# Optimization experiments

Hardware: AMD Instinct MI355X
Metric: run time of the kernel (lower is better)

## Reference

```python
import jax, jax.numpy as jnp
import numpy as np

B, D, T_STEPS = 256, 512, 64


def setup_inputs() -> dict:
    key = jax.random.key(0)
    ks = jax.random.split(key, 9)
    s = 1.0 / np.sqrt(D)  # torch LSTM init scale
    return {
        "h": jax.random.normal(ks[0], (B, D), dtype=jnp.float32),
        "T": T_STEPS,
        "W_ih0": jax.random.uniform(ks[1], (4 * D, D), jnp.float32, -s, s),
        "W_hh0": jax.random.uniform(ks[2], (4 * D, D), jnp.float32, -s, s),
        "b_ih0": jax.random.uniform(ks[3], (4 * D,), jnp.float32, -s, s),
        "b_hh0": jax.random.uniform(ks[4], (4 * D,), jnp.float32, -s, s),
        "W_ih1": jax.random.uniform(ks[5], (4 * D, D), jnp.float32, -s, s),
        "W_hh1": jax.random.uniform(ks[6], (4 * D, D), jnp.float32, -s, s),
        "b_ih1": jax.random.uniform(ks[7], (4 * D,), jnp.float32, -s, s),
        "b_hh1": jax.random.uniform(ks[8], (4 * D,), jnp.float32, -s, s),
    }


def _lstm_cell(x, h, c, W_ih, W_hh, b_ih, b_hh):
    # gates: [B, 4D], torch gate order (i, f, g, o)
    gates = x @ W_ih.T + h @ W_hh.T + (b_ih + b_hh)
    i, f, g, o = jnp.split(gates, 4, axis=-1)
    c_new = jax.nn.sigmoid(f) * c + jax.nn.sigmoid(i) * jnp.tanh(g)
    h_new = jax.nn.sigmoid(o) * jnp.tanh(c_new)
    return h_new, c_new


def reference(h, T, W_ih0, W_hh0, b_ih0, b_hh0, W_ih1, W_hh1, b_ih1, b_hh1):
    b, d = h.shape
    zeros = jnp.zeros((b, d), dtype=h.dtype)

    def step(carry, _):
        x, h0, c0, h1, c1 = carry
        h0, c0 = _lstm_cell(x, h0, c0, W_ih0, W_hh0, b_ih0, b_hh0)
        h1, c1 = _lstm_cell(h0, h1, c1, W_ih1, W_hh1, b_ih1, b_hh1)
        # output of layer 2 is fed back as next step's input
        return (h1, h0, c0, h1, c1), h1

    init = (h, zeros, zeros, zeros, zeros)
    _, e_seq = jax.lax.scan(step, init, xs=None, length=T)
    return e_seq  # [T, B, D]
```

## Files before the change

### kernel.cpp

```cpp
#include <hip/hip_runtime.h>


#define BD    131072
#define SMEM_WBYTES 131072
#define SMEM_BYTES  (SMEM_WBYTES + 4 * 1056 * 4)

#define WS_SLOTS 0
#define WS_XINIT 4096
#define WS_ZERO  (WS_XINIT + BD * 2)
#define WS_ROT   (WS_ZERO + BD * 2)
#define ROT_BYTES ((size_t)BD * 2)
#define WS_NEED_DEEP (WS_ROT + 128 * ROT_BYTES)
#define WS_NEED_RING (WS_ROT + 4 * ROT_BYTES)

typedef _Float16 half8_t  __attribute__((ext_vector_type(8)));
typedef float    f32x16_t __attribute__((ext_vector_type(16)));
typedef float    f32x4_t  __attribute__((ext_vector_type(4)));

#define LOADC(p)  __hip_atomic_load((p), __ATOMIC_RELAXED, __HIP_MEMORY_SCOPE_AGENT)
#define STOREC(p, v) __hip_atomic_store((p), (v), __ATOMIC_RELAXED, __HIP_MEMORY_SCOPE_AGENT)

__device__ __forceinline__ float sigmoidf_(float x) {
  float z = __expf(-fabsf(x));
  float s = 1.0f / (1.0f + z);
  return x >= 0.0f ? s : 1.0f - s;
}
__device__ __forceinline__ float tanhf_(float x) {
  float z = __expf(-2.0f * fabsf(x));
  float t = (1.0f - z) / (1.0f + z);
  return x >= 0.0f ? t : -t;
}

__device__ __forceinline__ f32x4_t load_cv16(const void* p) {
  f32x4_t r;
  asm volatile("global_load_dwordx4 %0, %1, off sc0 sc1"
               : "=v"(r) : "v"(p) : "memory");
  return r;
}

__global__ void lstm_init(const float* __restrict__ h, char* __restrict__ ws) {
  int i = blockIdx.x * 256 + threadIdx.x;
  unsigned* slots = (unsigned*)(ws + WS_SLOTS);
  _Float16* xinit = (_Float16*)(ws + WS_XINIT);
  _Float16* zerob = (_Float16*)(ws + WS_ZERO);
  if (i < BD) {
    xinit[i] = (_Float16)h[i];
    zerob[i] = (_Float16)0.0f;
  }
  if (i < 256) slots[i] = 0u;
}

__global__ void __launch_bounds__(256, 1) lstm_persist(
    const float* __restrict__ Wih0, const float* __restrict__ Whh0,
    const float* __restrict__ bih0, const float* __restrict__ bhh0,
    const float* __restrict__ Wih1, const float* __restrict__ Whh1,
    const float* __restrict__ bih1, const float* __restrict__ bhh1,
    float* __restrict__ out, char* __restrict__ ws, int deep)
{
  extern __shared__ char smem[];
  float* red = (float*)(smem + SMEM_WBYTES);
  unsigned* slots = (unsigned*)(ws + WS_SLOTS);
  const _Float16* xinit = (const _Float16*)(ws + WS_XINIT);
  const _Float16* zerob = (const _Float16*)(ws + WS_ZERO);
  char* rot = ws + WS_ROT;

  const int tid = threadIdx.x;
  const int l = tid & 63;
  const int w = tid >> 6;
  const int bid = blockIdx.x;
  const int bb = (bid & 7) >> 1;
  const int db = ((bid >> 3) << 1) | (bid & 1);
  const int b0 = bb << 6;
  const int d0 = db << 3;

#pragma unroll
  for (int L = 0; L < 2; ++L) {
    for (int it = 0; it < 16; ++it) {
      int slot = it * 256 + tid;
      int s2 = slot >> 6, lane = slot & 63;
      int khalf = s2 >> 5, ks = s2 & 31;
      int kg = lane >> 5, nl = lane & 31;
      int ng = ((nl >> 3) << 9) + d0 + (nl & 7);
      int col = ks * 16 + kg * 8;
      const float* srcb = khalf ? (L ? Whh1 : Whh0) : (L ? Wih1 : Wih0);
      const float* src = srcb + (size_t)ng * 512 + col;
      half8_t hv;
#pragma unroll
      for (int j = 0; j < 8; ++j) hv[j] = (_Float16)src[j];
      *(half8_t*)(smem + (size_t)L * 65536 + (size_t)slot * 16) = hv;
    }
  }

  const int cbl = tid >> 2;
  const int j0 = (tid & 3) << 1;
  float bias0[4][2], bias1[4][2];
#pragma unroll
  for (int g = 0; g < 4; ++g) {
#pragma unroll
    for (int p = 0; p < 2; ++p) {
      int ng = (g << 9) + d0 + j0 + p;
      bias0[g][p] = bih0[ng] + bhh0[ng];
      bias1[g][p] = bih1[ng] + bhh1[ng];
    }
  }
  float c0s[2] = {0.0f, 0.0f}, c1s[2] = {0.0f, 0.0f};
  unsigned* gflags = slots + (bb << 6);
  __syncthreads();

  for (int s = 0; s < 128; ++s) {
    const int t = s >> 1;
    const int layer = s & 1;
    const int fi = deep ? (s - 1) : ((s - 1) & 3);
    const int si = deep ? (s - 2) : ((s - 2) & 3);
    const int oi = deep ? s : (s & 3);
    const _Float16* fresh = (s == 0) ? xinit
                          : (const _Float16*)(rot + (size_t)fi * ROT_BYTES);
    const _Float16* stale = (s <= 1) ? zerob
                          : (const _Float16*)(rot + (size_t)si * ROT_BYTES);
    _Float16* hout = (_Float16*)(rot + (size_t)oi * ROT_BYTES);

    if (w < 2 && s > 0) {
      const unsigned* sl = gflags + l;
      unsigned v;
      do {
        v = LOADC(sl);
      } while (!__all((int)(v >= (unsigned)s)));
      asm volatile("" ::: "memory");
    }

    const _Float16* asrc = (w >= 2) ? stale : fresh;
    const char* ap = (const char*)(asrc + (size_t)(b0 + ((w & 1) << 5) + (l & 31)) * 512
                                        + ((l >> 5) << 3));
    int boff = layer * 65536 + ((w >> 1) * 32768) + l * 16;

    f32x16_t acc0, acc1;
#pragma unroll
    for (int r = 0; r < 16; ++r) { acc0[r] = 0.0f; acc1[r] = 0.0f; }

    if (deep) {
#pragma unroll
      for (int half = 0; half < 2; ++half) {
        f32x4_t va[16];
#pragma unroll
        for (int j = 0; j < 16; ++j)
          va[j] = *(const f32x4_t*)(ap + half * 512 + 32 * j);
#pragma unroll
        for (int ks = 0; ks < 8; ++ks) {
          half8_t a0  = __builtin_bit_cast(half8_t, va[2 * ks]);
          half8_t a1  = __builtin_bit_cast(half8_t, va[2 * ks + 1]);
          half8_t bv0 = *(const half8_t*)(smem + boff);
          half8_t bv1 = *(const half8_t*)(smem + boff + 1024);
          acc0 = __builtin_amdgcn_mfma_f32_32x32x16_f16(a0, bv0, acc0, 0, 0, 0);
          acc1 = __builtin_amdgcn_mfma_f32_32x32x16_f16(a1, bv1, acc1, 0, 0, 0);
          boff += 2048;
        }
      }
    } else {
#pragma unroll
      for (int half = 0; half < 2; ++half) {
        f32x4_t va[16];
#pragma unroll
        for (int j = 0; j < 16; ++j) va[j] = load_cv16(ap + half * 512 + 32 * j);
        asm volatile("s_waitcnt vmcnt(0)" ::: "memory");
#pragma unroll
        for (int ks = 0; ks < 8; ++ks) {
          half8_t a0  = __builtin_bit_cast(half8_t, va[2 * ks]);
          half8_t a1  = __builtin_bit_cast(half8_t, va[2 * ks + 1]);
          half8_t bv0 = *(const half8_t*)(smem + boff);
          half8_t bv1 = *(const half8_t*)(smem + boff + 1024);
          acc0 = __builtin_amdgcn_mfma_f32_32x32x16_f16(a0, bv0, acc0, 0, 0, 0);
          acc1 = __builtin_amdgcn_mfma_f32_32x32x16_f16(a1, bv1, acc1, 0, 0, 0);
          boff += 2048;
        }
      }
    }

    {
      float* redw = red + w * 1056 + (l & 31);
      const int rbase = (l >> 5) << 2;
#pragma unroll
      for (int r = 0; r < 16; ++r) {
        int row = (r & 3) + ((r >> 2) << 3) + rbase;
        redw[row * 33] = acc0[r] + acc1[r];
      }
    }
    __syncthreads();

    float hv[2];
    int gidx;
    {
      const int base = (cbl >> 5) * 1056 + (cbl & 31) * 33 + j0;
#pragma unroll
      for (int p = 0; p < 2; ++p) {
        float vi = red[base + p]      + red[base + 2112 + p]      + (layer ? bias1[0][p] : bias0[0][p]);
        float vf = red[base + 8 + p]  + red[base + 2112 + 8 + p]  + (layer ? bias1[1][p] : bias0[1][p]);
        float vg = red[base + 16 + p] + red[base + 2112 + 16 + p] + (layer ? bias1[2][p] : bias0[2][p]);
        float vo = red[base + 24 + p] + red[base + 2112 + 24 + p] + (layer ? bias1[3][p] : bias0[3][p]);
        float iv = sigmoidf_(vi), fv = sigmoidf_(vf);
        float gv = tanhf_(vg),    ov = sigmoidf_(vo);
        float cold = layer ? c1s[p] : c0s[p];
        float c = fv * cold + iv * gv;
        if (layer) c1s[p] = c; else c0s[p] = c;
        hv[p] = ov * tanhf_(c);
      }
      gidx = (b0 + cbl) * 512 + d0 + j0;
      unsigned hu = ((unsigned)__builtin_bit_cast(unsigned short, (_Float16)hv[0])) |
                    ((unsigned)__builtin_bit_cast(unsigned short, (_Float16)hv[1]) << 16);
      STOREC((unsigned*)&hout[gidx], hu);
    }
    asm volatile("s_waitcnt vmcnt(0)" ::: "memory");
    __syncthreads();
    if (tid == 0)
      STOREC(gflags + db, (unsigned)(s + 1));
    if (layer) {
      float* op = out + (size_t)t * BD + gidx;
      op[0] = hv[0]; op[1] = hv[1];
    }
  }
}

extern "C" void kernel_launch(void* const* d_in, const int* in_sizes, int n_in,
                              void* d_out, int out_size, void* d_ws, size_t ws_size,
                              hipStream_t stream) {
  const float* h    = (const float*)d_in[0];
  const float* Wih0 = (const float*)d_in[2];
  const float* Whh0 = (const float*)d_in[3];
  const float* bih0 = (const float*)d_in[4];
  const float* bhh0 = (const float*)d_in[5];
  const float* Wih1 = (const float*)d_in[6];
  const float* Whh1 = (const float*)d_in[7];
  const float* bih1 = (const float*)d_in[8];
  const float* bhh1 = (const float*)d_in[9];
  float* out = (float*)d_out;
  char* ws = (char*)d_ws;

  int deep = (ws_size >= (size_t)WS_NEED_DEEP) ? 1 : 0;

  hipFuncSetAttribute((const void*)lstm_persist,
                      hipFuncAttributeMaxDynamicSharedMemorySize, SMEM_BYTES);

  lstm_init<<<512, 256, 0, stream>>>(h, ws);

  void* args[] = { &Wih0, &Whh0, &bih0, &bhh0, &Wih1, &Whh1, &bih1, &bhh1,
                   &out, &ws, &deep };
  hipLaunchCooperativeKernel((void*)lstm_persist, dim3(256), dim3(256),
                             args, SMEM_BYTES, stream);
}
```

Baseline: 1.127 ms.

## Replace flag-based inter-block sync with sentinel-poisoned data polling

Drops the per-step flag counters and the spin-wait on them. The init kernel fills the whole 128-slot history buffer with an all-ones sentinel, and consumer waves poll the fresh h data itself until no word equals the sentinel. Each step therefore needs one round of global traffic instead of a flag store followed by a data load. The shallow ring-buffer fallback and the cooperative launch are removed. This relies on valid fp16 pairs never encoding 0xFFFFFFFF, adds an init pass that writes the full 32MB buffer, and skips work entirely if the workspace is too small.

```diff
diff --git a/kernel.cpp b/kernel.cpp
--- a/kernel.cpp
+++ b/kernel.cpp
@@ -5,19 +5,17 @@
 #define SMEM_WBYTES 131072
 #define SMEM_BYTES  (SMEM_WBYTES + 4 * 1056 * 4)
 
-#define WS_SLOTS 0
 #define WS_XINIT 4096
 #define WS_ZERO  (WS_XINIT + BD * 2)
 #define WS_ROT   (WS_ZERO + BD * 2)
 #define ROT_BYTES ((size_t)BD * 2)
-#define WS_NEED_DEEP (WS_ROT + 128 * ROT_BYTES)
-#define WS_NEED_RING (WS_ROT + 4 * ROT_BYTES)
+#define WS_NEED  (WS_ROT + 128 * ROT_BYTES)
 
 typedef _Float16 half8_t  __attribute__((ext_vector_type(8)));
 typedef float    f32x16_t __attribute__((ext_vector_type(16)));
 typedef float    f32x4_t  __attribute__((ext_vector_type(4)));
-
-#define LOADC(p)  __hip_atomic_load((p), __ATOMIC_RELAXED, __HIP_MEMORY_SCOPE_AGENT)
+typedef unsigned uint4_t  __attribute__((ext_vector_type(4)));
+
 #define STOREC(p, v) __hip_atomic_store((p), (v), __ATOMIC_RELAXED, __HIP_MEMORY_SCOPE_AGENT)
 
 __device__ __forceinline__ float sigmoidf_(float x) {
@@ -40,14 +38,16 @@
 
 __global__ void lstm_init(const float* __restrict__ h, char* __restrict__ ws) {
   int i = blockIdx.x * 256 + threadIdx.x;
-  unsigned* slots = (unsigned*)(ws + WS_SLOTS);
   _Float16* xinit = (_Float16*)(ws + WS_XINIT);
   _Float16* zerob = (_Float16*)(ws + WS_ZERO);
   if (i < BD) {
     xinit[i] = (_Float16)h[i];
     zerob[i] = (_Float16)0.0f;
   }
-  if (i < 256) slots[i] = 0u;
+  uint4_t* rot4 = (uint4_t*)(ws + WS_ROT);
+  uint4_t s4; s4[0] = 0xFFFFFFFFu; s4[1] = 0xFFFFFFFFu;
+  s4[2] = 0xFFFFFFFFu; s4[3] = 0xFFFFFFFFu;
+  for (int j = i; j < 2097152; j += 524288) rot4[j] = s4;
 }
 
 __global__ void __launch_bounds__(256, 1) lstm_persist(
@@ -55,11 +55,10 @@
     const float* __restrict__ bih0, const float* __restrict__ bhh0,
     const float* __restrict__ Wih1, const float* __restrict__ Whh1,
     const float* __restrict__ bih1, const float* __restrict__ bhh1,
-    float* __restrict__ out, char* __restrict__ ws, int deep)
+    float* __restrict__ out, char* __restrict__ ws)
 {
   extern __shared__ char smem[];
   float* red = (float*)(smem + SMEM_WBYTES);
-  unsigned* slots = (unsigned*)(ws + WS_SLOTS);
   const _Float16* xinit = (const _Float16*)(ws + WS_XINIT);
   const _Float16* zerob = (const _Float16*)(ws + WS_ZERO);
   char* rot = ws + WS_ROT;
@@ -104,74 +103,60 @@
     }
   }
   float c0s[2] = {0.0f, 0.0f}, c1s[2] = {0.0f, 0.0f};
-  unsigned* gflags = slots + (bb << 6);
   __syncthreads();
 
   for (int s = 0; s < 128; ++s) {
     const int t = s >> 1;
     const int layer = s & 1;
-    const int fi = deep ? (s - 1) : ((s - 1) & 3);
-    const int si = deep ? (s - 2) : ((s - 2) & 3);
-    const int oi = deep ? s : (s & 3);
     const _Float16* fresh = (s == 0) ? xinit
-                          : (const _Float16*)(rot + (size_t)fi * ROT_BYTES);
+                          : (const _Float16*)(rot + (size_t)(s - 1) * ROT_BYTES);
     const _Float16* stale = (s <= 1) ? zerob
-                          : (const _Float16*)(rot + (size_t)si * ROT_BYTES);
-    _Float16* hout = (_Float16*)(rot + (size_t)oi * ROT_BYTES);
-
-    if (w < 2 && s > 0) {
-      const unsigned* sl = gflags + l;
-      unsigned v;
-      do {
-        v = LOADC(sl);
-      } while (!__all((int)(v >= (unsigned)s)));
-      asm volatile("" ::: "memory");
-    }
+                          : (const _Float16*)(rot + (size_t)(s - 2) * ROT_BYTES);
+    _Float16* hout = (_Float16*)(rot + (size_t)s * ROT_BYTES);
 
     const _Float16* asrc = (w >= 2) ? stale : fresh;
     const char* ap = (const char*)(asrc + (size_t)(b0 + ((w & 1) << 5) + (l & 31)) * 512
                                         + ((l >> 5) << 3));
+    const bool needcheck = (w < 2) && (s > 0);
     int boff = layer * 65536 + ((w >> 1) * 32768) + l * 16;
 
     f32x16_t acc0, acc1;
 #pragma unroll
     for (int r = 0; r < 16; ++r) { acc0[r] = 0.0f; acc1[r] = 0.0f; }
 
-    if (deep) {
-#pragma unroll
-      for (int half = 0; half < 2; ++half) {
-        f32x4_t va[16];
-#pragma unroll
-        for (int j = 0; j < 16; ++j)
-          va[j] = *(const f32x4_t*)(ap + half * 512 + 32 * j);
-#pragma unroll
-        for (int ks = 0; ks < 8; ++ks) {
-          half8_t a0  = __builtin_bit_cast(half8_t, va[2 * ks]);
-          half8_t a1  = __builtin_bit_cast(half8_t, va[2 * ks + 1]);
-          half8_t bv0 = *(const half8_t*)(smem + boff);
-          half8_t bv1 = *(const half8_t*)(smem + boff + 1024);
-          acc0 = __builtin_amdgcn_mfma_f32_32x32x16_f16(a0, bv0, acc0, 0, 0, 0);
-          acc1 = __builtin_amdgcn_mfma_f32_32x32x16_f16(a1, bv1, acc1, 0, 0, 0);
-          boff += 2048;
+#pragma unroll
+    for (int half = 0; half < 2; ++half) {
+      f32x4_t va[16];
+      if (needcheck) {
+        while (true) {
+#pragma unroll
+          for (int j = 0; j < 16; ++j) va[j] = load_cv16(ap + half * 512 + 32 * j);
+          asm volatile("s_waitcnt vmcnt(0)" ::: "memory");
+          unsigned mx = 0u;
+#pragma unroll
+          for (int j = 0; j < 16; ++j)
+#pragma unroll
+            for (int d = 0; d < 4; ++d) {
+              unsigned u = __float_as_uint(va[j][d]);
+              mx = (u > mx) ? u : mx;
+            }
+          if (__all(mx != 0xFFFFFFFFu)) break;
+          asm volatile("s_sleep 2");
         }
-      }
-    } else {
-#pragma unroll
-      for (int half = 0; half < 2; ++half) {
-        f32x4_t va[16];
+      } else {
 #pragma unroll
         for (int j = 0; j < 16; ++j) va[j] = load_cv16(ap + half * 512 + 32 * j);
         asm volatile("s_waitcnt vmcnt(0)" ::: "memory");
-#pragma unroll
-        for (int ks = 0; ks < 8; ++ks) {
-          half8_t a0  = __builtin_bit_cast(half8_t, va[2 * ks]);
-          half8_t a1  = __builtin_bit_cast(half8_t, va[2 * ks + 1]);
-          half8_t bv0 = *(const half8_t*)(smem + boff);
-          half8_t bv1 = *(const half8_t*)(smem + boff + 1024);
-          acc0 = __builtin_amdgcn_mfma_f32_32x32x16_f16(a0, bv0, acc0, 0, 0, 0);
-          acc1 = __builtin_amdgcn_mfma_f32_32x32x16_f16(a1, bv1, acc1, 0, 0, 0);
-          boff += 2048;
-        }
+      }
+#pragma unroll
+      for (int ks = 0; ks < 8; ++ks) {
+        half8_t a0  = __builtin_bit_cast(half8_t, va[2 * ks]);
+        half8_t a1  = __builtin_bit_cast(half8_t, va[2 * ks + 1]);
+        half8_t bv0 = *(const half8_t*)(smem + boff);
+        half8_t bv1 = *(const half8_t*)(smem + boff + 1024);
+        acc0 = __builtin_amdgcn_mfma_f32_32x32x16_f16(a0, bv0, acc0, 0, 0, 0);
+        acc1 = __builtin_amdgcn_mfma_f32_32x32x16_f16(a1, bv1, acc1, 0, 0, 0);
+        boff += 2048;
       }
     }
 
@@ -186,10 +171,9 @@
     }
     __syncthreads();
 
-    float hv[2];
-    int gidx;
     {
       const int base = (cbl >> 5) * 1056 + (cbl & 31) * 33 + j0;
+      float hv[2];
 #pragma unroll
       for (int p = 0; p < 2; ++p) {
         float vi = red[base + p]      + red[base + 2112 + p]      + (layer ? bias1[0][p] : bias0[0][p]);
@@ -203,19 +187,16 @@
         if (layer) c1s[p] = c; else c0s[p] = c;
         hv[p] = ov * tanhf_(c);
       }
-      gidx = (b0 + cbl) * 512 + d0 + j0;
+      const int gidx = (b0 + cbl) * 512 + d0 + j0;
       unsigned hu = ((unsigned)__builtin_bit_cast(unsigned short, (_Float16)hv[0])) |
                     ((unsigned)__builtin_bit_cast(unsigned short, (_Float16)hv[1]) << 16);
       STOREC((unsigned*)&hout[gidx], hu);
-    }
-    asm volatile("s_waitcnt vmcnt(0)" ::: "memory");
+      if (layer) {
+        float* op = out + (size_t)t * BD + gidx;
+        op[0] = hv[0]; op[1] = hv[1];
+      }
+    }
     __syncthreads();
-    if (tid == 0)
-      STOREC(gflags + db, (unsigned)(s + 1));
-    if (layer) {
-      float* op = out + (size_t)t * BD + gidx;
-      op[0] = hv[0]; op[1] = hv[1];
-    }
   }
 }
 
@@ -234,15 +215,14 @@
   float* out = (float*)d_out;
   char* ws = (char*)d_ws;
 
-  int deep = (ws_size >= (size_t)WS_NEED_DEEP) ? 1 : 0;
+  if (ws_size < (size_t)WS_NEED) return;
 
   hipFuncSetAttribute((const void*)lstm_persist,
                       hipFuncAttributeMaxDynamicSharedMemorySize, SMEM_BYTES);
 
-  lstm_init<<<512, 256, 0, stream>>>(h, ws);
-
-  void* args[] = { &Wih0, &Whh0, &bih0, &bhh0, &Wih1, &Whh1, &bih1, &bhh1,
-                   &out, &ws, &deep };
-  hipLaunchCooperativeKernel((void*)lstm_persist, dim3(256), dim3(256),
-                             args, SMEM_BYTES, stream);
-}
+  lstm_init<<<2048, 256, 0, stream>>>(h, ws);
+
+  lstm_persist<<<256, 256, SMEM_BYTES, stream>>>(Wih0, Whh0, bih0, bhh0,
+                                                 Wih1, Whh1, bih1, bhh1,
+                                                 out, ws);
+}
```

Result: faster. 921.5 us (-18.2%).
